# Optimization experiments

Measured on AMD Instinct MI355X. Metric: run time of the kernel, lower is better.

The kernel has to match this reference:

```python
import jax, jax.numpy as jnp
import numpy as np

BOUND = np.array([[-4.0, 4.0], [-4.0, 4.0], [-2.0, 2.0]], dtype=np.float32)
N_PTS = 1048576
PLANE_C = 3
PLANE_RES = [128, 256, 512, 1024]
N_LEVELS = 16
F_PER = 2
T = 2 ** 16  # hashmap size (log2_hashmap_size=16)
BASE_RES = 16
FINEST = int(float((BOUND[:, 1] - BOUND[:, 0]).max()) / 0.02)  # 400
_growth = np.exp(np.log(FINEST / BASE_RES) / (N_LEVELS - 1))
HASH_RES = np.floor(BASE_RES * _growth ** np.arange(N_LEVELS)).astype(np.float32)
PRIMES = jnp.array([1, 2654435761, 805459861], dtype=jnp.uint32)


def setup_inputs() -> dict:
    key = jax.random.key(0)
    ks = jax.random.split(key, 32)
    lo = jnp.asarray(BOUND[:, 0]); hi = jnp.asarray(BOUND[:, 1])
    inp = {}
    inp['p'] = jax.random.uniform(ks[0], (N_PTS, 3), dtype=jnp.float32) * (hi - lo) + lo
    i = 1
    for li, r in enumerate(PLANE_RES):
        for name in ('xy', 'xz', 'yz'):
            inp[f'plane_{name}_{li}'] = 0.1 * jax.random.normal(ks[i], (PLANE_C, r, r), dtype=jnp.float32)
            i += 1
    inp['hash_table'] = jax.random.uniform(ks[i], (N_LEVELS, T, F_PER), dtype=jnp.float32, minval=-1e-4, maxval=1e-4); i += 1

    def lin(k, fi, fo):
        s = 1.0 / np.sqrt(fi)
        k1, k2 = jax.random.split(k)
        return (jax.random.uniform(k1, (fi, fo), minval=-s, maxval=s, dtype=jnp.float32),
                jax.random.uniform(k2, (fo,), minval=-s, maxval=s, dtype=jnp.float32))

    c_in = 12 * PLANE_C + N_LEVELS * F_PER  # 68
    inp['W0'], inp['b0'] = lin(ks[i], c_in, 64); i += 1
    inp['W1'], inp['b1'] = lin(ks[i], 64, 64); i += 1
    inp['Wo'], inp['bo'] = lin(ks[i], 64, 33); i += 1  # 1 sdf + 32 geo_feat
    inp['Wc0'], inp['bc0'] = lin(ks[i], 12 * PLANE_C + 32, 64); i += 1
    inp['Wc1'], inp['bc1'] = lin(ks[i], 64, 32); i += 1
    inp['Wco'], inp['bco'] = lin(ks[i], 32, 3); i += 1
    return inp


def sample_plane(plane, u, v):
    """Bilinear grid_sample, align_corners=True, padding_mode='border'.
    plane: (C,H,W); u indexes W, v indexes H; u,v in [-1,1]. Returns (N,C)."""
    C, H, W = plane.shape
    x = jnp.clip((u + 1.0) * 0.5 * (W - 1), 0.0, W - 1)
    y = jnp.clip((v + 1.0) * 0.5 * (H - 1), 0.0, H - 1)
    x0 = jnp.floor(x); y0 = jnp.floor(y)
    wx = x - x0; wy = y - y0
    x0i = x0.astype(jnp.int32); y0i = y0.astype(jnp.int32)
    x1i = jnp.minimum(x0i + 1, W - 1); y1i = jnp.minimum(y0i + 1, H - 1)
    g = lambda yi, xi: plane[:, yi, xi]  # (C,N)
    out = (g(y0i, x0i) * ((1 - wy) * (1 - wx)) + g(y0i, x1i) * ((1 - wy) * wx)
           + g(y1i, x0i) * (wy * (1 - wx)) + g(y1i, x1i) * (wy * wx))
    return out.T


def hash_encode(p01, table):
    """Multi-res hash grid (instant-ngp style). p01: (N,3) in [0,1]; table: (L,T,F) -> (N, L*F)."""
    res = jnp.asarray(HASH_RES)  # (L,)

    def level(r, tab):
        x = p01 * r
        x0 = jnp.floor(x)
        w = x - x0
        xi = x0.astype(jnp.uint32)  # (N,3)
        feat = jnp.zeros((p01.shape[0], F_PER), dtype=table.dtype)
        for dz in (0, 1):
            for dy in (0, 1):
                for dx in (0, 1):
                    c = xi + jnp.array([dx, dy, dz], dtype=jnp.uint32)
                    h = c * PRIMES[None, :]
                    idx = ((h[:, 0] ^ h[:, 1] ^ h[:, 2]) % T).astype(jnp.int32)
                    wgt = ((w[:, 0] if dx else 1 - w[:, 0])
                           * (w[:, 1] if dy else 1 - w[:, 1])
                           * (w[:, 2] if dz else 1 - w[:, 2]))
                    feat = feat + tab[idx] * wgt[:, None]
        return feat  # (N,F)

    feats = jax.vmap(level, in_axes=(0, 0))(res, table)  # (L,N,F)
    return jnp.transpose(feats, (1, 0, 2)).reshape(p01.shape[0], N_LEVELS * F_PER)


def _forward(p, plane_xy_0, plane_xz_0, plane_yz_0, plane_xy_1, plane_xz_1, plane_yz_1,
             plane_xy_2, plane_xz_2, plane_yz_2, plane_xy_3, plane_xz_3, plane_yz_3,
             hash_table, W0, b0, W1, b1, Wo, bo, Wc0, bc0, Wc1, bc1, Wco, bco):
    bound = jnp.asarray(BOUND)
    p_nor = (p - bound[:, 0]) / (bound[:, 1] - bound[:, 0]) * 2.0 - 1.0  # normalize_3d_coordinate
    u, v, w = p_nor[:, 0], p_nor[:, 1], p_nor[:, 2]
    levels = [(plane_xy_0, plane_xz_0, plane_yz_0), (plane_xy_1, plane_xz_1, plane_yz_1),
              (plane_xy_2, plane_xz_2, plane_yz_2), (plane_xy_3, plane_xz_3, plane_yz_3)]
    feats = []
    for pxy, pxz, pyz in levels:
        feats += [sample_plane(pxy, u, v), sample_plane(pxz, u, w), sample_plane(pyz, v, w)]
    plane_feat = jnp.concatenate(feats, axis=-1)  # (N, 36)
    hfeat = hash_encode((p_nor + 1.0) * 0.5, hash_table)  # (N, 32)
    # SDF branch
    h = jnp.concatenate([plane_feat, hfeat], axis=-1)  # (N, 68)
    h = jax.nn.relu(h @ W0 + b0)
    h = jax.nn.relu(h @ W1 + b1)
    sf = jnp.tanh(h @ Wo + bo)
    sdf, geo_feat = sf[:, :1], sf[:, 1:]
    # RGB branch
    c = jnp.concatenate([geo_feat, plane_feat], axis=-1)  # (N, 68)
    c = jax.nn.relu(c @ Wc0 + bc0)
    c = jax.nn.relu(c @ Wc1 + bc1)
    rgb = jax.nn.sigmoid(c @ Wco + bco)
    return jnp.concatenate([rgb, sdf], axis=-1)  # (N, 4)


def reference(p, plane_xy_0, plane_xz_0, plane_yz_0, plane_xy_1, plane_xz_1, plane_yz_1,
              plane_xy_2, plane_xz_2, plane_yz_2, plane_xy_3, plane_xz_3, plane_yz_3,
              hash_table, W0, b0, W1, b1, Wo, bo, Wc0, bc0, Wc1, bc1, Wco, bco):
    return _forward(p, plane_xy_0, plane_xz_0, plane_yz_0, plane_xy_1, plane_xz_1, plane_yz_1,
                    plane_xy_2, plane_xz_2, plane_yz_2, plane_xy_3, plane_xz_3, plane_yz_3,
                    hash_table, W0, b0, W1, b1, Wo, bo, Wc0, bc0, Wc1, bc1, Wco, bco)
```

## Files before the change

### kernel.cpp

```cpp
#include <hip/hip_runtime.h>

#define NPTS 1048576
#define NBKT 262144

typedef short bhalf8 __attribute__((ext_vector_type(8)));
typedef float floatx4 __attribute__((ext_vector_type(4)));

#define WSZ 24320
#define FROWS 21
#define MLP_THREADS 1024
#define MLP_WAVES 16

#define PB_PLANES 16320
#define PB_HASH 4096
#define PB_HIST 4096

__device__ const float HRg[16] = {16.f, 19.f, 24.f, 30.f, 37.f, 46.f, 57.f, 71.f,
                                  89.f, 110.f, 136.f, 169.f, 210.f, 260.f, 322.f, 400.f};


__device__ __forceinline__ float my_tanh(float x) {
  float e = __expf(2.f * x);
  return 1.f - 2.f * __builtin_amdgcn_rcpf(e + 1.f);
}

__device__ __forceinline__ float my_sigmoid(float x) {
  return __builtin_amdgcn_rcpf(1.f + __expf(-x));
}

__device__ __forceinline__ unsigned short bf16rne(float v) {
  unsigned u = __float_as_uint(v);
  unsigned r = (u + 0x7fffu + ((u >> 16) & 1u)) >> 16;
  return (unsigned short)r;
}

__device__ __forceinline__ float texch(uint2 t, int c) {
  unsigned u = (c == 0) ? (t.x << 16) : (c == 1) ? (t.x & 0xffff0000u) : (t.y << 16);
  return __uint_as_float(u);
}

__device__ __forceinline__ float bflo(unsigned u) { return __uint_as_float(u << 16); }
__device__ __forceinline__ float bfhi(unsigned u) { return __uint_as_float(u & 0xffff0000u); }

__device__ __forceinline__ unsigned mort6(unsigned x) {
  return (x & 1) | ((x & 2) << 2) | ((x & 4) << 4) |
         ((x & 8) << 6) | ((x & 16) << 8) | ((x & 32) << 10);
}

__device__ __forceinline__ unsigned morton_key(float px, float py, float pz) {
  float qx = (px + 4.f) * 0.125f, qy = (py + 4.f) * 0.125f, qz = (pz + 2.f) * 0.25f;
  unsigned kx = min(63, max(0, (int)(qx * 64.f)));
  unsigned ky = min(63, max(0, (int)(qy * 64.f)));
  unsigned kz = min(63, max(0, (int)(qz * 64.f)));
  return mort6(kx) | (mort6(ky) << 1) | (mort6(kz) << 2);
}

__device__ __forceinline__ unsigned hash_level(const unsigned* __restrict__ ht, int lv,
                                               float q0, float q1, float q2) {
  const float r = HRg[lv];
  float x0 = q0 * r, x1 = q1 * r, x2 = q2 * r;
  float f0 = floorf(x0), f1 = floorf(x1), f2 = floorf(x2);
  float w0 = x0 - f0, w1 = x1 - f1, w2 = x2 - f2;
  unsigned i0 = (unsigned)(int)f0, i1 = (unsigned)(int)f1, i2 = (unsigned)(int)f2;
  const unsigned* __restrict__ hb = ht + ((unsigned)lv << 16);
  unsigned tv[8];
#pragma unroll
  for (int dz = 0; dz < 2; ++dz)
#pragma unroll
    for (int dy = 0; dy < 2; ++dy)
#pragma unroll
      for (int dx = 0; dx < 2; ++dx) {
        unsigned h = (i0 + dx) ^ ((i1 + dy) * 2654435761u) ^ ((i2 + dz) * 805459861u);
        tv[dz * 4 + dy * 2 + dx] = hb[h & 65535u];
      }
  float a0 = 0.f, a1 = 0.f;
#pragma unroll
  for (int c = 0; c < 8; ++c) {
    const int dx = c & 1, dy = (c >> 1) & 1, dz = c >> 2;
    float wgt = (dx ? w0 : 1.f - w0) * (dy ? w1 : 1.f - w1) * (dz ? w2 : 1.f - w2);
    a0 = fmaf(bflo(tv[c]), wgt, a0);
    a1 = fmaf(bfhi(tv[c]), wgt, a1);
  }
  return (unsigned)bf16rne(a0) | ((unsigned)bf16rne(a1) << 16);
}


struct PrepParams {
  const float* psrc[12];
  ushort4* pdst[12];
  const float* hash;
  unsigned* hashb;
  const float* p;
  unsigned* hist;
};

__global__ __launch_bounds__(256) void prep_kernel(PrepParams P) {
  const int b = blockIdx.x;
  if (b < PB_PLANES) {
    const int CUM[13] = {0, 16384, 32768, 49152, 114688, 180224, 245760,
                         507904, 770048, 1032192, 2080768, 3129344, 4177920};
    const int RESL[12] = {128, 128, 128, 256, 256, 256, 512, 512, 512, 1024, 1024, 1024};
    const int s = b << 8;
    int pi = 0;
#pragma unroll
    for (int i = 1; i < 12; ++i)
      if (s >= CUM[i]) pi = i;
    const int li = s + threadIdx.x - CUM[pi];
    const int R = RESL[pi];
    const int n = R * R;
    const float* __restrict__ src = P.psrc[pi];
    ushort4 t;
    t.x = bf16rne(src[li]);
    t.y = bf16rne(src[n + li]);
    t.z = bf16rne(src[2 * n + li]);
    t.w = 0;
    P.pdst[pi][li] = t;
  } else if (b < PB_PLANES + PB_HASH) {
    const int i = ((b - PB_PLANES) << 8) + threadIdx.x;
    float2 v = *(const float2*)(P.hash + (size_t)i * 2);
    P.hashb[i] = (unsigned)bf16rne(v.x) | ((unsigned)bf16rne(v.y) << 16);
  } else {
    const int i = ((b - PB_PLANES - PB_HASH) << 8) + threadIdx.x;
    const float* pp = P.p + (size_t)i * 3;
    unsigned k = morton_key(pp[0], pp[1], pp[2]);
    atomicAdd(&P.hist[k], 1u);
  }
}


__global__ __launch_bounds__(256) void scan1_kernel(const unsigned* __restrict__ hist,
                                                    unsigned* __restrict__ partial) {
  __shared__ unsigned s[256];
  const int b = blockIdx.x, t = threadIdx.x;
  uint4 v = ((const uint4*)(hist + b * 1024))[t];
  s[t] = v.x + v.y + v.z + v.w;
  __syncthreads();
  for (int d = 128; d > 0; d >>= 1) {
    if (t < d) s[t] += s[t + d];
    __syncthreads();
  }
  if (t == 0) partial[b] = s[0];
}

__global__ __launch_bounds__(256) void scan2_kernel(const unsigned* __restrict__ partial,
                                                    unsigned* __restrict__ base) {
  __shared__ unsigned s[256];
  const int t = threadIdx.x;
  s[t] = partial[t];
  __syncthreads();
  for (int d = 1; d < 256; d <<= 1) {
    unsigned v = (t >= d) ? s[t - d] : 0u;
    __syncthreads();
    s[t] += v;
    __syncthreads();
  }
  base[t] = (t == 0) ? 0u : s[t - 1];
}

__global__ __launch_bounds__(256) void scan3_kernel(const unsigned* __restrict__ hist,
                                                    const unsigned* __restrict__ base,
                                                    unsigned* __restrict__ cursor) {
  __shared__ unsigned s[256];
  const int b = blockIdx.x, t = threadIdx.x;
  uint4 v = ((const uint4*)(hist + b * 1024))[t];
  unsigned sum = v.x + v.y + v.z + v.w;
  s[t] = sum;
  __syncthreads();
  for (int d = 1; d < 256; d <<= 1) {
    unsigned x = (t >= d) ? s[t - d] : 0u;
    __syncthreads();
    s[t] += x;
    __syncthreads();
  }
  unsigned off = base[b] + s[t] - sum;
  uint4 c;
  c.x = off;
  c.y = off + v.x;
  c.z = off + v.x + v.y;
  c.w = off + v.x + v.y + v.z;
  ((uint4*)(cursor + b * 1024))[t] = c;
}

__global__ __launch_bounds__(256) void scatter_kernel(const float* __restrict__ p,
                                                      unsigned* __restrict__ cursor,
                                                      unsigned* __restrict__ perm) {
  int i = blockIdx.x * 256 + threadIdx.x;
  const float* pp = p + (size_t)i * 3;
  unsigned k = morton_key(pp[0], pp[1], pp[2]);
  unsigned slot = atomicAdd(&cursor[k], 1u);
  perm[slot] = (unsigned)i;
}


__global__ __launch_bounds__(256) void repack_plane(const float* __restrict__ src,
                                                    ushort4* __restrict__ dst, int R) {
  int i = blockIdx.x * 256 + threadIdx.x;
  int n = R * R;
  if (i >= n) return;
  ushort4 t;
  t.x = bf16rne(src[i]);
  t.y = bf16rne(src[n + i]);
  t.z = bf16rne(src[2 * n + i]);
  t.w = 0;
  dst[i] = t;
}


__device__ __forceinline__ void sample3i(const uint2* __restrict__ pl,
                                         float a, float b, int R, float* f) {
  const float Rm1 = (float)(R - 1);
  float x = fminf(fmaxf((a + 1.f) * 0.5f * Rm1, 0.f), Rm1);
  float y = fminf(fmaxf((b + 1.f) * 0.5f * Rm1, 0.f), Rm1);
  float x0f = floorf(x), y0f = floorf(y);
  float wx = x - x0f, wy = y - y0f;
  int x0 = (int)x0f, y0 = (int)y0f;
  int x1 = min(x0 + 1, R - 1), y1 = min(y0 + 1, R - 1);
  float w00 = (1.f - wy) * (1.f - wx);
  float w01 = (1.f - wy) * wx;
  float w10 = wy * (1.f - wx);
  float w11 = wy * wx;
  uint2 t00 = pl[y0 * R + x0];
  uint2 t01 = pl[y0 * R + x1];
  uint2 t10 = pl[y1 * R + x0];
  uint2 t11 = pl[y1 * R + x1];
#pragma unroll
  for (int c = 0; c < 3; ++c) {
    f[c] = texch(t00, c) * w00 + texch(t01, c) * w01 +
           texch(t10, c) * w10 + texch(t11, c) * w11;
  }
}

__device__ __forceinline__ void sample3f(const float* __restrict__ pl,
                                         float a, float b, int R, float* f) {
  const float Rm1 = (float)(R - 1);
  float x = fminf(fmaxf((a + 1.f) * 0.5f * Rm1, 0.f), Rm1);
  float y = fminf(fmaxf((b + 1.f) * 0.5f * Rm1, 0.f), Rm1);
  float x0f = floorf(x), y0f = floorf(y);
  float wx = x - x0f, wy = y - y0f;
  int x0 = (int)x0f, y0 = (int)y0f;
  int x1 = min(x0 + 1, R - 1), y1 = min(y0 + 1, R - 1);
  float w00 = (1.f - wy) * (1.f - wx);
  float w01 = (1.f - wy) * wx;
  float w10 = wy * (1.f - wx);
  float w11 = wy * wx;
  int i00 = y0 * R + x0, i01 = y0 * R + x1;
  int i10 = y1 * R + x0, i11 = y1 * R + x1;
  const int R2 = R * R;
#pragma unroll
  for (int c = 0; c < 3; ++c) {
    const float* base = pl + c * R2;
    f[c] = base[i00] * w00 + base[i01] * w01 + base[i10] * w10 + base[i11] * w11;
  }
}


struct FeatParams {
  const float* p;
  const uint2* pli[12];
  const unsigned* perm;
  unsigned* fbuf;
};

template <bool SORT>
__global__ __launch_bounds__(256) void feat_kernel(FeatParams P) {
  int bid = blockIdx.x;
  if (SORT) bid = (bid & 7) * (NPTS / 256 / 8) + (bid >> 3);
  const int tid = bid * 256 + threadIdx.x;
  const int pid = SORT ? (int)P.perm[tid] : tid;

  const float* __restrict__ pp = P.p + (size_t)pid * 3;
  const float px = pp[0], py = pp[1], pz = pp[2];

  const float u = (px + 4.f) * 0.25f - 1.f;
  const float v = (py + 4.f) * 0.25f - 1.f;
  const float w = (pz + 2.f) * 0.5f - 1.f;

  float pf[36];
  {
    const int RES[4] = {128, 256, 512, 1024};
#pragma unroll
    for (int li = 0; li < 4; ++li) {
      sample3i(P.pli[li * 3 + 0], u, v, RES[li], &pf[li * 9 + 0]);
      sample3i(P.pli[li * 3 + 1], u, w, RES[li], &pf[li * 9 + 3]);
      sample3i(P.pli[li * 3 + 2], v, w, RES[li], &pf[li * 9 + 6]);
    }
  }
  unsigned* __restrict__ F = P.fbuf;
#pragma unroll
  for (int kk = 0; kk < 18; ++kk) {
    unsigned pk = (unsigned)bf16rne(pf[2 * kk]) | ((unsigned)bf16rne(pf[2 * kk + 1]) << 16);
    F[(size_t)kk * NPTS + tid] = pk;
  }
  F[(size_t)18 * NPTS + tid] = __float_as_uint((px + 4.f) * 0.125f);
  F[(size_t)19 * NPTS + tid] = __float_as_uint((py + 4.f) * 0.125f);
  F[(size_t)20 * NPTS + tid] = __float_as_uint((pz + 2.f) * 0.25f);
}


struct MlpWParams {
  const unsigned* fbuf;
  const unsigned* perm;
  const unsigned* hashb;
  const float* W0; const float* b0;
  const float* W1; const float* b1;
  const float* Wo; const float* bo;
  const float* Wc0; const float* bc0;
  const float* Wc1; const float* bc1;
  const float* Wco; const float* bco;
  float* out;
};

__device__ __forceinline__ void stage_w(const float* __restrict__ src, int K, int Nsrc,
                                        int STR, int NPAD, int OFF, short* Wlds, int tid) {
  const int total = NPAD * STR;
  for (int idx = tid; idx < total; idx += MLP_THREADS) {
    int c = idx / STR;
    int k = idx - c * STR;
    float val = (k < K && c < Nsrc) ? src[k * Nsrc + c] : 0.f;
    unsigned short hi = bf16rne(val);
    float hif = __uint_as_float((unsigned)hi << 16);
    unsigned short lo = bf16rne(val - hif);
    Wlds[OFF + idx] = (short)hi;
    Wlds[WSZ + OFF + idx] = (short)lo;
  }
}

__device__ __forceinline__ void stage_b(const float* __restrict__ src, int Nsrc, int NPAD,
                                        int BOFF, float* Blds, int tid) {
  for (int j = tid; j < NPAD; j += MLP_THREADS) Blds[BOFF + j] = (j < Nsrc) ? src[j] : 0.f;
}

__device__ __forceinline__ bhalf8 ldA(const unsigned* __restrict__ fbuf, int pt,
                                      int kkBase, int kkLim) {
  bhalf8 r;
#pragma unroll
  for (int j = 0; j < 4; ++j) {
    const int kk = kkBase + j;
    unsigned d = 0u;
    if (kk < kkLim) d = fbuf[(size_t)kk * NPTS + pt];
    r[2 * j] = (short)(d & 0xffffu);
    r[2 * j + 1] = (short)(d >> 16);
  }
  return r;
}

__device__ __forceinline__ bhalf8 frag4(unsigned d0, unsigned d1, unsigned d2, unsigned d3) {
  bhalf8 r;
  r[0] = (short)(d0 & 0xffffu); r[1] = (short)(d0 >> 16);
  r[2] = (short)(d1 & 0xffffu); r[3] = (short)(d1 >> 16);
  r[4] = (short)(d2 & 0xffffu); r[5] = (short)(d2 >> 16);
  r[6] = (short)(d3 & 0xffffu); r[7] = (short)(d3 >> 16);
  return r;
}

__device__ __forceinline__ bhalf8 ldS(const short* scr, int rowl, int grp, int s) {
  return *(const bhalf8*)&scr[rowl * 72 + 32 * s + 8 * grp];
}

template <int NT, int KS, int OFF, int STR>
__device__ __forceinline__ void mlayer(const bhalf8 (&af)[KS], floatx4 (&acc)[NT],
                                       const short* Wlds, int rowl, int grp) {
#pragma unroll
  for (int n = 0; n < NT; ++n) {
    floatx4 a{};
#pragma unroll
    for (int s = 0; s < KS; ++s) {
      const int wo = OFF + (16 * n + rowl) * STR + 32 * s + 8 * grp;
      const bhalf8 bh = *(const bhalf8*)&Wlds[wo];
      a = __builtin_amdgcn_mfma_f32_16x16x32_bf16(af[s], bh, a, 0, 0, 0);
      const bhalf8 bl = *(const bhalf8*)&Wlds[WSZ + wo];
      a = __builtin_amdgcn_mfma_f32_16x16x32_bf16(af[s], bl, a, 0, 0, 0);
    }
    acc[n] = a;
  }
}

template <int NT>
__device__ __forceinline__ void relu_wr(const floatx4 (&acc)[NT], const float* Blds,
                                        int boff, short* scr, int rowl, int grp) {
#pragma unroll
  for (int n = 0; n < NT; ++n) {
    const float b = Blds[boff + 16 * n + rowl];
#pragma unroll
    for (int r = 0; r < 4; ++r) {
      float v = fmaxf(acc[n][r] + b, 0.f);
      scr[(grp * 4 + r) * 72 + 16 * n + rowl] = (short)bf16rne(v);
    }
  }
}

__device__ __forceinline__ void tanh_wr(const floatx4 (&acc)[3], const float* Blds,
                                        short* scr, float* ost, int rowl, int grp) {
#pragma unroll
  for (int n = 0; n < 3; ++n) {
    const float b = Blds[128 + 16 * n + rowl];
    const int c = 16 * n + rowl;
#pragma unroll
    for (int r = 0; r < 4; ++r) {
      float v = my_tanh(acc[n][r] + b);
      if (n == 0 && rowl == 0) ost[(grp * 4 + r) * 4 + 3] = v;
      if (c >= 1 && c <= 32) scr[(grp * 4 + r) * 72 + c - 1] = (short)bf16rne(v);
    }
  }
}

template <bool SORT>
__global__ __launch_bounds__(MLP_THREADS) void mlp_mfma(MlpWParams P) {
  __shared__ short Wlds[2 * WSZ];
  __shared__ float Blds[288];
  __shared__ short Scr[MLP_WAVES * 16 * 72];
  __shared__ float Ost[MLP_WAVES][16][4];

  const int tid = threadIdx.x;

  stage_w(P.W0,  68, 64, 104, 64,     0, Wlds, tid);
  stage_w(P.W1,  64, 64,  72, 64,  6656, Wlds, tid);
  stage_w(P.Wo,  64, 33,  72, 48, 11264, Wlds, tid);
  stage_w(P.Wc0, 68, 64, 104, 64, 14720, Wlds, tid);
  stage_w(P.Wc1, 64, 32,  72, 32, 21376, Wlds, tid);
  stage_w(P.Wco, 32,  3,  40, 16, 23680, Wlds, tid);
  stage_b(P.b0,  64, 64,   0, Blds, tid);
  stage_b(P.b1,  64, 64,  64, Blds, tid);
  stage_b(P.bo,  33, 48, 128, Blds, tid);
  stage_b(P.bc0, 64, 64, 176, Blds, tid);
  stage_b(P.bc1, 32, 32, 240, Blds, tid);
  stage_b(P.bco,  3, 16, 272, Blds, tid);
  __syncthreads();

  const int wave = tid >> 6, lane = tid & 63;
  const int rowl = lane & 15, grp = lane >> 4;
  short* scr0 = &Scr[wave * 16 * 72];
  float* ost0 = &Ost[wave][0][0];

  const int lv0 = (grp == 0) ? 0 : (4 * grp - 2);

  for (int t = 0; t < 8; ++t) {
    const int wbase = ((blockIdx.x * 8 + t) * MLP_WAVES + wave) * 16;
    const int ptA = wbase + rowl;

    {
      const unsigned* __restrict__ F = P.fbuf;
      float qA0 = __uint_as_float(F[(size_t)18 * NPTS + ptA]);
      float qA1 = __uint_as_float(F[(size_t)19 * NPTS + ptA]);
      float qA2 = __uint_as_float(F[(size_t)20 * NPTS + ptA]);

      unsigned hA0, hA1, hA2, hA3;
      {
        const int l0 = lv0, l1 = lv0 + 1;
        const int l2 = (grp == 0) ? 14 : (lv0 + 2);
        const int l3 = (grp == 0) ? 15 : (lv0 + 3);
        hA0 = hash_level(P.hashb, l0, qA0, qA1, qA2);
        hA1 = hash_level(P.hashb, l1, qA0, qA1, qA2);
        hA2 = hash_level(P.hashb, l2, qA0, qA1, qA2);
        hA3 = hash_level(P.hashb, l3, qA0, qA1, qA2);
      }

      unsigned pA16 = F[(size_t)16 * NPTS + ptA], pA17 = F[(size_t)17 * NPTS + ptA];

      bhalf8 s1A = (grp == 0) ? frag4(pA16, pA17, hA0, hA1) : frag4(hA0, hA1, hA2, hA3);
      bhalf8 s2A = (grp == 0) ? frag4(hA2, hA3, 0u, 0u) : frag4(0u, 0u, 0u, 0u);

      bhalf8 afA[3] = {ldA(P.fbuf, ptA, 4 * grp, 18), s1A, s2A};
      floatx4 accA[4];
      mlayer<4, 3, 0, 104>(afA, accA, Wlds, rowl, grp);
      relu_wr<4>(accA, Blds, 0, scr0, rowl, grp);
    }
    {
      bhalf8 afA[2] = {ldS(scr0, rowl, grp, 0), ldS(scr0, rowl, grp, 1)};
      floatx4 accA[4];
      mlayer<4, 2, 6656, 72>(afA, accA, Wlds, rowl, grp);
      relu_wr<4>(accA, Blds, 64, scr0, rowl, grp);
    }
    {
      bhalf8 afA[2] = {ldS(scr0, rowl, grp, 0), ldS(scr0, rowl, grp, 1)};
      floatx4 accA[3];
      mlayer<3, 2, 11264, 72>(afA, accA, Wlds, rowl, grp);
      tanh_wr(accA, Blds, scr0, ost0, rowl, grp);
    }
    {
      bhalf8 afA[3] = {ldS(scr0, rowl, grp, 0),
                       ldA(P.fbuf, ptA, 0 + 4 * grp, 18),
                       ldA(P.fbuf, ptA, 16 + 4 * grp, 18)};
      floatx4 accA[4];
      mlayer<4, 3, 14720, 104>(afA, accA, Wlds, rowl, grp);
      relu_wr<4>(accA, Blds, 176, scr0, rowl, grp);
    }
    {
      bhalf8 afA[2] = {ldS(scr0, rowl, grp, 0), ldS(scr0, rowl, grp, 1)};
      floatx4 accA[2];
      mlayer<2, 2, 21376, 72>(afA, accA, Wlds, rowl, grp);
      relu_wr<2>(accA, Blds, 240, scr0, rowl, grp);
    }
    {
      bhalf8 afA[1] = {ldS(scr0, rowl, grp, 0)};
      floatx4 accA[1];
      mlayer<1, 1, 23680, 40>(afA, accA, Wlds, rowl, grp);
      const float b = Blds[272 + rowl];
#pragma unroll
      for (int r = 0; r < 4; ++r) {
        float vA = my_sigmoid(accA[0][r] + b);
        if (rowl < 3) ost0[(grp * 4 + r) * 4 + rowl] = vA;
      }
    }

    if (lane < 16) {
      float4 o = *(float4*)&Ost[wave][lane][0];
      int dst = SORT ? (int)P.perm[wbase + lane] : (wbase + lane);
      ((float4*)P.out)[dst] = o;
    }
  }
}


struct DecParams {
  const float* p;
  const float* pl[12];
  const uint2* pli[12];
  const float* hash;
  const float* W0; const float* b0;
  const float* W1; const float* b1;
  const float* Wo; const float* bo;
  const float* Wc0; const float* bc0;
  const float* Wc1; const float* bc1;
  const float* Wco; const float* bco;
  float* out;
};

template <bool ILV>
__global__ __launch_bounds__(256) void dec_kernel(DecParams P) {
  const int tid = blockIdx.x * 256 + threadIdx.x;

  const float* __restrict__ pp = P.p + (size_t)tid * 3;
  const float px = pp[0], py = pp[1], pz = pp[2];

  const float u = (px + 4.f) * 0.25f - 1.f;
  const float v = (py + 4.f) * 0.25f - 1.f;
  const float w = (pz + 2.f) * 0.5f - 1.f;

  float feat[68];
  {
    const int RES[4] = {128, 256, 512, 1024};
#pragma unroll
    for (int li = 0; li < 4; ++li) {
      if (ILV) {
        sample3i(P.pli[li * 3 + 0], u, v, RES[li], &feat[li * 9 + 0]);
        sample3i(P.pli[li * 3 + 1], u, w, RES[li], &feat[li * 9 + 3]);
        sample3i(P.pli[li * 3 + 2], v, w, RES[li], &feat[li * 9 + 6]);
      } else {
        sample3f(P.pl[li * 3 + 0], u, v, RES[li], &feat[li * 9 + 0]);
        sample3f(P.pl[li * 3 + 1], u, w, RES[li], &feat[li * 9 + 3]);
        sample3f(P.pl[li * 3 + 2], v, w, RES[li], &feat[li * 9 + 6]);
      }
    }
  }

  {
    const float q0 = (px + 4.f) * 0.125f;
    const float q1 = (py + 4.f) * 0.125f;
    const float q2 = (pz + 2.f) * 0.25f;
    const float* __restrict__ ht = P.hash;
#pragma unroll
    for (int l = 0; l < 16; ++l) {
      const float r = HRg[l];
      float x0 = q0 * r, x1 = q1 * r, x2 = q2 * r;
      float f0 = floorf(x0), f1 = floorf(x1), f2 = floorf(x2);
      float w0 = x0 - f0, w1 = x1 - f1, w2 = x2 - f2;
      unsigned i0 = (unsigned)(int)f0, i1 = (unsigned)(int)f1, i2 = (unsigned)(int)f2;
      float a0 = 0.f, a1 = 0.f;
#pragma unroll
      for (int dz = 0; dz < 2; ++dz)
#pragma unroll
        for (int dy = 0; dy < 2; ++dy)
#pragma unroll
          for (int dx = 0; dx < 2; ++dx) {
            unsigned h = (i0 + dx) ^ ((i1 + dy) * 2654435761u) ^ ((i2 + dz) * 805459861u);
            unsigned idx = h & 65535u;
            const float2 tv = *(const float2*)(ht + (((unsigned)l << 16) + idx) * 2);
            float wgt = (dx ? w0 : 1.f - w0) * (dy ? w1 : 1.f - w1) * (dz ? w2 : 1.f - w2);
            a0 = fmaf(tv.x, wgt, a0);
            a1 = fmaf(tv.y, wgt, a1);
          }
      feat[36 + l * 2] = a0;
      feat[36 + l * 2 + 1] = a1;
    }
  }

  float acc[64];
#pragma unroll
  for (int j = 0; j < 64; ++j) acc[j] = P.b0[j];
#pragma unroll
  for (int i = 0; i < 68; ++i) {
    const float a = feat[i];
    const float* wr = P.W0 + i * 64;
#pragma unroll
    for (int j = 0; j < 64; ++j) acc[j] = fmaf(a, wr[j], acc[j]);
  }
  float hid[64];
#pragma unroll
  for (int j = 0; j < 64; ++j) hid[j] = fmaxf(acc[j], 0.f);

#pragma unroll
  for (int j = 0; j < 64; ++j) acc[j] = P.b1[j];
#pragma unroll
  for (int i = 0; i < 64; ++i) {
    const float a = hid[i];
    const float* wr = P.W1 + i * 64;
#pragma unroll
    for (int j = 0; j < 64; ++j) acc[j] = fmaf(a, wr[j], acc[j]);
  }
#pragma unroll
  for (int j = 0; j < 64; ++j) hid[j] = fmaxf(acc[j], 0.f);

  float so[33];
#pragma unroll
  for (int j = 0; j < 33; ++j) so[j] = P.bo[j];
#pragma unroll
  for (int i = 0; i < 64; ++i) {
    const float a = hid[i];
    const float* wr = P.Wo + i * 33;
#pragma unroll
    for (int j = 0; j < 33; ++j) so[j] = fmaf(a, wr[j], so[j]);
  }
  const float sdf = my_tanh(so[0]);
  float geo[32];
#pragma unroll
  for (int j = 0; j < 32; ++j) geo[j] = my_tanh(so[j + 1]);

#pragma unroll
  for (int j = 0; j < 64; ++j) acc[j] = P.bc0[j];
#pragma unroll
  for (int i = 0; i < 32; ++i) {
    const float a = geo[i];
    const float* wr = P.Wc0 + i * 64;
#pragma unroll
    for (int j = 0; j < 64; ++j) acc[j] = fmaf(a, wr[j], acc[j]);
  }
#pragma unroll
  for (int i = 0; i < 36; ++i) {
    const float a = feat[i];
    const float* wr = P.Wc0 + (32 + i) * 64;
#pragma unroll
    for (int j = 0; j < 64; ++j) acc[j] = fmaf(a, wr[j], acc[j]);
  }
#pragma unroll
  for (int j = 0; j < 64; ++j) hid[j] = fmaxf(acc[j], 0.f);

  float c1[32];
#pragma unroll
  for (int j = 0; j < 32; ++j) c1[j] = P.bc1[j];
#pragma unroll
  for (int i = 0; i < 64; ++i) {
    const float a = hid[i];
    const float* wr = P.Wc1 + i * 32;
#pragma unroll
    for (int j = 0; j < 32; ++j) c1[j] = fmaf(a, wr[j], c1[j]);
  }

  float r0 = P.bco[0], r1 = P.bco[1], r2 = P.bco[2];
#pragma unroll
  for (int i = 0; i < 32; ++i) {
    const float a = fmaxf(c1[i], 0.f);
    r0 = fmaf(a, P.Wco[i * 3 + 0], r0);
    r1 = fmaf(a, P.Wco[i * 3 + 1], r1);
    r2 = fmaf(a, P.Wco[i * 3 + 2], r2);
  }

  float4 o;
  o.x = my_sigmoid(r0);
  o.y = my_sigmoid(r1);
  o.z = my_sigmoid(r2);
  o.w = sdf;
  ((float4*)P.out)[tid] = o;
}


extern "C" void kernel_launch(void* const* d_in, const int* in_sizes, int n_in,
                              void* d_out, int out_size, void* d_ws, size_t ws_size,
                              hipStream_t stream) {
  const int RES[4] = {128, 256, 512, 1024};
  const size_t planes_bytes = (size_t)3 * (128 * 128 + 256 * 256 + 512 * 512 + 1024 * 1024) * 8;
  const size_t hash_bytes = (size_t)16 * 65536 * 4;
  const size_t feat_bytes = (size_t)FROWS * NPTS * 4;
  const size_t perm_bytes = (size_t)NPTS * 4;
  const size_t hist_bytes = (size_t)NBKT * 4;
  const size_t need_full = planes_bytes + hash_bytes + feat_bytes + 64;
  const size_t need_sort = need_full + perm_bytes + 2 * hist_bytes + 4096;
  const size_t need_mid = planes_bytes + 64;

  char* wsp = (char*)d_ws;
  const float* p = (const float*)d_in[0];

  if (ws_size >= need_sort) {
    size_t off = 0;
    PrepParams PP;
    PP.p = p;
    PP.hash = (const float*)d_in[13];
    const uint2* pli[12];
    for (int i = 0; i < 12; ++i) {
      int R = RES[i / 3];
      PP.psrc[i] = (const float*)d_in[1 + i];
      PP.pdst[i] = (ushort4*)(wsp + off);
      pli[i] = (const uint2*)(wsp + off);
      off += (size_t)R * R * 8;
    }
    unsigned* hashb = (unsigned*)(wsp + off);
    PP.hashb = hashb;
    off += hash_bytes;
    unsigned* fbuf = (unsigned*)(wsp + off);
    off += feat_bytes;
    unsigned* perm = (unsigned*)(wsp + off);
    off += perm_bytes;
    unsigned* hist = (unsigned*)(wsp + off);
    off += hist_bytes;
    unsigned* cursor = (unsigned*)(wsp + off);
    off += hist_bytes;
    unsigned* partial = (unsigned*)(wsp + off);
    off += 1024;
    unsigned* base = (unsigned*)(wsp + off);
    off += 1024;
    PP.hist = hist;

    hipMemsetAsync(hist, 0, hist_bytes, stream);
    prep_kernel<<<PB_PLANES + PB_HASH + PB_HIST, 256, 0, stream>>>(PP);
    scan1_kernel<<<256, 256, 0, stream>>>(hist, partial);
    scan2_kernel<<<1, 256, 0, stream>>>(partial, base);
    scan3_kernel<<<256, 256, 0, stream>>>(hist, base, cursor);
    scatter_kernel<<<NPTS / 256, 256, 0, stream>>>(p, cursor, perm);

    FeatParams FP;
    FP.p = p;
    for (int i = 0; i < 12; ++i) FP.pli[i] = pli[i];
    FP.perm = perm;
    FP.fbuf = fbuf;
    feat_kernel<true><<<NPTS / 256, 256, 0, stream>>>(FP);

    MlpWParams MP;
    MP.fbuf = fbuf;
    MP.perm = perm;
    MP.hashb = hashb;
    MP.W0 = (const float*)d_in[14]; MP.b0 = (const float*)d_in[15];
    MP.W1 = (const float*)d_in[16]; MP.b1 = (const float*)d_in[17];
    MP.Wo = (const float*)d_in[18]; MP.bo = (const float*)d_in[19];
    MP.Wc0 = (const float*)d_in[20]; MP.bc0 = (const float*)d_in[21];
    MP.Wc1 = (const float*)d_in[22]; MP.bc1 = (const float*)d_in[23];
    MP.Wco = (const float*)d_in[24]; MP.bco = (const float*)d_in[25];
    MP.out = (float*)d_out;
    mlp_mfma<true><<<512, MLP_THREADS, 0, stream>>>(MP);
    return;
  }

  if (ws_size >= need_full) {
    size_t off = 0;
    PrepParams PP;
    PP.p = p;
    PP.hash = (const float*)d_in[13];
    const uint2* pli[12];
    for (int i = 0; i < 12; ++i) {
      int R = RES[i / 3];
      PP.psrc[i] = (const float*)d_in[1 + i];
      PP.pdst[i] = (ushort4*)(wsp + off);
      pli[i] = (const uint2*)(wsp + off);
      off += (size_t)R * R * 8;
    }
    unsigned* hashb = (unsigned*)(wsp + off);
    PP.hashb = hashb;
    off += hash_bytes;
    unsigned* fbuf = (unsigned*)(wsp + off);
    PP.hist = nullptr;

    prep_kernel<<<PB_PLANES + PB_HASH, 256, 0, stream>>>(PP);

    FeatParams FP;
    FP.p = p;
    for (int i = 0; i < 12; ++i) FP.pli[i] = pli[i];
    FP.perm = nullptr;
    FP.fbuf = fbuf;
    feat_kernel<false><<<NPTS / 256, 256, 0, stream>>>(FP);

    MlpWParams MP;
    MP.fbuf = fbuf;
    MP.perm = nullptr;
    MP.hashb = hashb;
    MP.W0 = (const float*)d_in[14]; MP.b0 = (const float*)d_in[15];
    MP.W1 = (const float*)d_in[16]; MP.b1 = (const float*)d_in[17];
    MP.Wo = (const float*)d_in[18]; MP.bo = (const float*)d_in[19];
    MP.Wc0 = (const float*)d_in[20]; MP.bc0 = (const float*)d_in[21];
    MP.Wc1 = (const float*)d_in[22]; MP.bc1 = (const float*)d_in[23];
    MP.Wco = (const float*)d_in[24]; MP.bco = (const float*)d_in[25];
    MP.out = (float*)d_out;
    mlp_mfma<false><<<512, MLP_THREADS, 0, stream>>>(MP);
    return;
  }

  DecParams P;
  P.p = p;
  for (int i = 0; i < 12; ++i) P.pl[i] = (const float*)d_in[1 + i];
  P.hash = (const float*)d_in[13];
  P.W0  = (const float*)d_in[14]; P.b0  = (const float*)d_in[15];
  P.W1  = (const float*)d_in[16]; P.b1  = (const float*)d_in[17];
  P.Wo  = (const float*)d_in[18]; P.bo  = (const float*)d_in[19];
  P.Wc0 = (const float*)d_in[20]; P.bc0 = (const float*)d_in[21];
  P.Wc1 = (const float*)d_in[22]; P.bc1 = (const float*)d_in[23];
  P.Wco = (const float*)d_in[24]; P.bco = (const float*)d_in[25];
  P.out = (float*)d_out;

  if (ws_size >= need_mid) {
    size_t off = 0;
    for (int i = 0; i < 12; ++i) {
      int R = RES[i / 3];
      int n = R * R;
      P.pli[i] = (const uint2*)(wsp + off);
      repack_plane<<<(n + 255) / 256, 256, 0, stream>>>(
          (const float*)d_in[1 + i], (ushort4*)(wsp + off), R);
      off += (size_t)n * 8;
    }
    dec_kernel<true><<<NPTS / 256, 256, 0, stream>>>(P);
  } else {
    for (int i = 0; i < 12; ++i) P.pli[i] = nullptr;
    dec_kernel<false><<<NPTS / 256, 256, 0, stream>>>(P);
  }
}
```

Before: 434.8 us.

## Switch storage and MFMA from bf16 with hi/lo weight split to fp16

Converts all packed planes, hash table, features and activations from bf16 to fp16. The MLP weights were split into bf16 hi and lo parts needing two MFMAs each; they are now a single fp16 copy with one f16 MFMA, halving matrix instructions and weight LDS. Conversions now use hardware half casts instead of manual rounding. The risk is fp16 range and precision limits, for example tiny hash values near 1e-4 lose mantissa bits.

```diff
diff --git a/kernel.cpp b/kernel.cpp
--- a/kernel.cpp
+++ b/kernel.cpp
@@ -4,6 +4,7 @@
 #define NBKT 262144
 
 typedef short bhalf8 __attribute__((ext_vector_type(8)));
+typedef _Float16 halfv8 __attribute__((ext_vector_type(8)));
 typedef float floatx4 __attribute__((ext_vector_type(4)));
 
 #define WSZ 24320
@@ -28,19 +29,25 @@
   return __builtin_amdgcn_rcpf(1.f + __expf(-x));
 }
 
-__device__ __forceinline__ unsigned short bf16rne(float v) {
-  unsigned u = __float_as_uint(v);
-  unsigned r = (u + 0x7fffu + ((u >> 16) & 1u)) >> 16;
-  return (unsigned short)r;
+__device__ __forceinline__ unsigned short f2h(float v) {
+  _Float16 h = (_Float16)v;
+  unsigned short u;
+  __builtin_memcpy(&u, &h, 2);
+  return u;
+}
+
+__device__ __forceinline__ float h2f(unsigned short u) {
+  _Float16 h;
+  __builtin_memcpy(&h, &u, 2);
+  return (float)h;
 }
 
 __device__ __forceinline__ float texch(uint2 t, int c) {
-  unsigned u = (c == 0) ? (t.x << 16) : (c == 1) ? (t.x & 0xffff0000u) : (t.y << 16);
-  return __uint_as_float(u);
-}
-
-__device__ __forceinline__ float bflo(unsigned u) { return __uint_as_float(u << 16); }
-__device__ __forceinline__ float bfhi(unsigned u) { return __uint_as_float(u & 0xffff0000u); }
+  unsigned short u = (c == 0) ? (unsigned short)(t.x & 0xffffu)
+                   : (c == 1) ? (unsigned short)(t.x >> 16)
+                              : (unsigned short)(t.y & 0xffffu);
+  return h2f(u);
+}
 
 __device__ __forceinline__ unsigned mort6(unsigned x) {
   return (x & 1) | ((x & 2) << 2) | ((x & 4) << 4) |
@@ -78,10 +85,10 @@
   for (int c = 0; c < 8; ++c) {
     const int dx = c & 1, dy = (c >> 1) & 1, dz = c >> 2;
     float wgt = (dx ? w0 : 1.f - w0) * (dy ? w1 : 1.f - w1) * (dz ? w2 : 1.f - w2);
-    a0 = fmaf(bflo(tv[c]), wgt, a0);
-    a1 = fmaf(bfhi(tv[c]), wgt, a1);
-  }
-  return (unsigned)bf16rne(a0) | ((unsigned)bf16rne(a1) << 16);
+    a0 = fmaf(h2f((unsigned short)(tv[c] & 0xffffu)), wgt, a0);
+    a1 = fmaf(h2f((unsigned short)(tv[c] >> 16)), wgt, a1);
+  }
+  return (unsigned)f2h(a0) | ((unsigned)f2h(a1) << 16);
 }
 
 
@@ -110,15 +117,15 @@
     const int n = R * R;
     const float* __restrict__ src = P.psrc[pi];
     ushort4 t;
-    t.x = bf16rne(src[li]);
-    t.y = bf16rne(src[n + li]);
-    t.z = bf16rne(src[2 * n + li]);
+    t.x = f2h(src[li]);
+    t.y = f2h(src[n + li]);
+    t.z = f2h(src[2 * n + li]);
     t.w = 0;
     P.pdst[pi][li] = t;
   } else if (b < PB_PLANES + PB_HASH) {
     const int i = ((b - PB_PLANES) << 8) + threadIdx.x;
     float2 v = *(const float2*)(P.hash + (size_t)i * 2);
-    P.hashb[i] = (unsigned)bf16rne(v.x) | ((unsigned)bf16rne(v.y) << 16);
+    P.hashb[i] = (unsigned)f2h(v.x) | ((unsigned)f2h(v.y) << 16);
   } else {
     const int i = ((b - PB_PLANES - PB_HASH) << 8) + threadIdx.x;
     const float* pp = P.p + (size_t)i * 3;
@@ -198,9 +205,9 @@
   int n = R * R;
   if (i >= n) return;
   ushort4 t;
-  t.x = bf16rne(src[i]);
-  t.y = bf16rne(src[n + i]);
-  t.z = bf16rne(src[2 * n + i]);
+  t.x = f2h(src[i]);
+  t.y = f2h(src[n + i]);
+  t.z = f2h(src[2 * n + i]);
   t.w = 0;
   dst[i] = t;
 }
@@ -288,7 +295,7 @@
   unsigned* __restrict__ F = P.fbuf;
 #pragma unroll
   for (int kk = 0; kk < 18; ++kk) {
-    unsigned pk = (unsigned)bf16rne(pf[2 * kk]) | ((unsigned)bf16rne(pf[2 * kk + 1]) << 16);
+    unsigned pk = (unsigned)f2h(pf[2 * kk]) | ((unsigned)f2h(pf[2 * kk + 1]) << 16);
     F[(size_t)kk * NPTS + tid] = pk;
   }
   F[(size_t)18 * NPTS + tid] = __float_as_uint((px + 4.f) * 0.125f);
@@ -317,11 +324,7 @@
     int c = idx / STR;
     int k = idx - c * STR;
     float val = (k < K && c < Nsrc) ? src[k * Nsrc + c] : 0.f;
-    unsigned short hi = bf16rne(val);
-    float hif = __uint_as_float((unsigned)hi << 16);
-    unsigned short lo = bf16rne(val - hif);
-    Wlds[OFF + idx] = (short)hi;
-    Wlds[WSZ + OFF + idx] = (short)lo;
+    Wlds[OFF + idx] = (short)f2h(val);
   }
 }
 
@@ -330,7 +333,13 @@
   for (int j = tid; j < NPAD; j += MLP_THREADS) Blds[BOFF + j] = (j < Nsrc) ? src[j] : 0.f;
 }
 
-__device__ __forceinline__ bhalf8 ldA(const unsigned* __restrict__ fbuf, int pt,
+__device__ __forceinline__ halfv8 as_h8(bhalf8 s) {
+  halfv8 h;
+  __builtin_memcpy(&h, &s, 16);
+  return h;
+}
+
+__device__ __forceinline__ halfv8 ldA(const unsigned* __restrict__ fbuf, int pt,
                                       int kkBase, int kkLim) {
   bhalf8 r;
 #pragma unroll
@@ -341,24 +350,24 @@
     r[2 * j] = (short)(d & 0xffffu);
     r[2 * j + 1] = (short)(d >> 16);
   }
-  return r;
-}
-
-__device__ __forceinline__ bhalf8 frag4(unsigned d0, unsigned d1, unsigned d2, unsigned d3) {
+  return as_h8(r);
+}
+
+__device__ __forceinline__ halfv8 frag4(unsigned d0, unsigned d1, unsigned d2, unsigned d3) {
   bhalf8 r;
   r[0] = (short)(d0 & 0xffffu); r[1] = (short)(d0 >> 16);
   r[2] = (short)(d1 & 0xffffu); r[3] = (short)(d1 >> 16);
   r[4] = (short)(d2 & 0xffffu); r[5] = (short)(d2 >> 16);
   r[6] = (short)(d3 & 0xffffu); r[7] = (short)(d3 >> 16);
-  return r;
-}
-
-__device__ __forceinline__ bhalf8 ldS(const short* scr, int rowl, int grp, int s) {
-  return *(const bhalf8*)&scr[rowl * 72 + 32 * s + 8 * grp];
+  return as_h8(r);
+}
+
+__device__ __forceinline__ halfv8 ldS(const short* scr, int rowl, int grp, int s) {
+  return *(const halfv8*)&scr[rowl * 72 + 32 * s + 8 * grp];
 }
 
 template <int NT, int KS, int OFF, int STR>
-__device__ __forceinline__ void mlayer(const bhalf8 (&af)[KS], floatx4 (&acc)[NT],
+__device__ __forceinline__ void mlayer(const halfv8 (&af)[KS], floatx4 (&acc)[NT],
                                        const short* Wlds, int rowl, int grp) {
 #pragma unroll
   for (int n = 0; n < NT; ++n) {
@@ -366,10 +375,8 @@
 #pragma unroll
     for (int s = 0; s < KS; ++s) {
       const int wo = OFF + (16 * n + rowl) * STR + 32 * s + 8 * grp;
-      const bhalf8 bh = *(const bhalf8*)&Wlds[wo];
-      a = __builtin_amdgcn_mfma_f32_16x16x32_bf16(af[s], bh, a, 0, 0, 0);
-      const bhalf8 bl = *(const bhalf8*)&Wlds[WSZ + wo];
-      a = __builtin_amdgcn_mfma_f32_16x16x32_bf16(af[s], bl, a, 0, 0, 0);
+      const halfv8 bh = *(const halfv8*)&Wlds[wo];
+      a = __builtin_amdgcn_mfma_f32_16x16x32_f16(af[s], bh, a, 0, 0, 0);
     }
     acc[n] = a;
   }
@@ -384,7 +391,7 @@
 #pragma unroll
     for (int r = 0; r < 4; ++r) {
       float v = fmaxf(acc[n][r] + b, 0.f);
-      scr[(grp * 4 + r) * 72 + 16 * n + rowl] = (short)bf16rne(v);
+      scr[(grp * 4 + r) * 72 + 16 * n + rowl] = (short)f2h(v);
     }
   }
 }
@@ -399,14 +406,14 @@
     for (int r = 0; r < 4; ++r) {
       float v = my_tanh(acc[n][r] + b);
       if (n == 0 && rowl == 0) ost[(grp * 4 + r) * 4 + 3] = v;
-      if (c >= 1 && c <= 32) scr[(grp * 4 + r) * 72 + c - 1] = (short)bf16rne(v);
+      if (c >= 1 && c <= 32) scr[(grp * 4 + r) * 72 + c - 1] = (short)f2h(v);
     }
   }
 }
 
 template <bool SORT>
 __global__ __launch_bounds__(MLP_THREADS) void mlp_mfma(MlpWParams P) {
-  __shared__ short Wlds[2 * WSZ];
+  __shared__ short Wlds[WSZ];
   __shared__ float Blds[288];
   __shared__ short Scr[MLP_WAVES * 16 * 72];
   __shared__ float Ost[MLP_WAVES][16][4];
@@ -457,28 +464,28 @@
 
       unsigned pA16 = F[(size_t)16 * NPTS + ptA], pA17 = F[(size_t)17 * NPTS + ptA];
 
-      bhalf8 s1A = (grp == 0) ? frag4(pA16, pA17, hA0, hA1) : frag4(hA0, hA1, hA2, hA3);
-      bhalf8 s2A = (grp == 0) ? frag4(hA2, hA3, 0u, 0u) : frag4(0u, 0u, 0u, 0u);
-
-      bhalf8 afA[3] = {ldA(P.fbuf, ptA, 4 * grp, 18), s1A, s2A};
+      halfv8 s1A = (grp == 0) ? frag4(pA16, pA17, hA0, hA1) : frag4(hA0, hA1, hA2, hA3);
+      halfv8 s2A = (grp == 0) ? frag4(hA2, hA3, 0u, 0u) : frag4(0u, 0u, 0u, 0u);
+
+      halfv8 afA[3] = {ldA(P.fbuf, ptA, 4 * grp, 18), s1A, s2A};
       floatx4 accA[4];
       mlayer<4, 3, 0, 104>(afA, accA, Wlds, rowl, grp);
       relu_wr<4>(accA, Blds, 0, scr0, rowl, grp);
     }
     {
-      bhalf8 afA[2] = {ldS(scr0, rowl, grp, 0), ldS(scr0, rowl, grp, 1)};
+      halfv8 afA[2] = {ldS(scr0, rowl, grp, 0), ldS(scr0, rowl, grp, 1)};
       floatx4 accA[4];
       mlayer<4, 2, 6656, 72>(afA, accA, Wlds, rowl, grp);
       relu_wr<4>(accA, Blds, 64, scr0, rowl, grp);
     }
     {
-      bhalf8 afA[2] = {ldS(scr0, rowl, grp, 0), ldS(scr0, rowl, grp, 1)};
+      halfv8 afA[2] = {ldS(scr0, rowl, grp, 0), ldS(scr0, rowl, grp, 1)};
       floatx4 accA[3];
       mlayer<3, 2, 11264, 72>(afA, accA, Wlds, rowl, grp);
       tanh_wr(accA, Blds, scr0, ost0, rowl, grp);
     }
     {
-      bhalf8 afA[3] = {ldS(scr0, rowl, grp, 0),
+      halfv8 afA[3] = {ldS(scr0, rowl, grp, 0),
                        ldA(P.fbuf, ptA, 0 + 4 * grp, 18),
                        ldA(P.fbuf, ptA, 16 + 4 * grp, 18)};
       floatx4 accA[4];
@@ -486,13 +493,13 @@
       relu_wr<4>(accA, Blds, 176, scr0, rowl, grp);
     }
     {
-      bhalf8 afA[2] = {ldS(scr0, rowl, grp, 0), ldS(scr0, rowl, grp, 1)};
+      halfv8 afA[2] = {ldS(scr0, rowl, grp, 0), ldS(scr0, rowl, grp, 1)};
       floatx4 accA[2];
       mlayer<2, 2, 21376, 72>(afA, accA, Wlds, rowl, grp);
       relu_wr<2>(accA, Blds, 240, scr0, rowl, grp);
     }
     {
-      bhalf8 afA[1] = {ldS(scr0, rowl, grp, 0)};
+      halfv8 afA[1] = {ldS(scr0, rowl, grp, 0)};
       floatx4 accA[1];
       mlayer<1, 1, 23680, 40>(afA, accA, Wlds, rowl, grp);
       const float b = Blds[272 + rowl];
```

After: 399.7 us. 8.1% less time.
